# Performance work log

Measured on AMD Instinct MI355X. Metric: run time of the kernel, lower is better.

## Reference

```python
import jax, jax.numpy as jnp
import numpy as np

NUM_CODEBOOKS = 1
NUM_ENTRIES = 4096
ENTRY_DIM = 64


def setup_inputs() -> dict:
    key = jax.random.key(0)
    k1, k2 = jax.random.split(key)
    z = jax.random.normal(k1, (4, 1024, 8, 64), dtype=jnp.float32)
    weight = jax.random.normal(k2, (NUM_CODEBOOKS * NUM_ENTRIES, ENTRY_DIM), dtype=jnp.float32)
    return {"z": z, "weight": weight}


def _decode(z, weight):
    # Mirrors VQVAEQuantize.decode with cosine_distance=False.
    C, K, D = NUM_CODEBOOKS, NUM_ENTRIES, ENTRY_DIM
    input_shape = z.shape
    zf = z.reshape(-1, C, D).astype(jnp.float32)            # (N, C, D)
    cb = weight.reshape(C, K, D).astype(jnp.float32)        # (C, K, D)
    dots = jnp.einsum('ckd,ncd->cnk', cb, zf)               # (C, N, K)
    znorm = jnp.sum(zf * zf, axis=-1).T[:, :, None]         # (C, N, 1)
    cbnorm = jnp.sum(cb * cb, axis=-1)[:, None, :]          # (C, 1, K)
    sim = 2.0 * dots - znorm - cbnorm                        # negative squared dist
    idx = jnp.argmax(sim, axis=-1)                           # (C, N)
    idx = idx.T + jnp.arange(C, dtype=idx.dtype)[None, :] * K  # (N, C) global ids
    idx = idx.reshape(*input_shape[:-1], -1)
    z_q = weight[idx.reshape(-1)].reshape(input_shape)       # embedding gather
    return z_q, idx


def reference(z, weight):
    z_q, indices = _decode(z, weight)
    # commitment loss (training path): mse per (bsz, seq_len) position
    commitment_loss = ((z - jax.lax.stop_gradient(z_q)) ** 2)
    commitment_loss = commitment_loss.reshape(z.shape[0], z.shape[1], -1).mean(axis=-1)
    # codebook EMA statistics (update_codebook): one-hot scatter-add as segment_sum
    K_total = NUM_CODEBOOKS * NUM_ENTRIES
    flat_idx = indices.reshape(-1)
    encodings_sum = jax.ops.segment_sum(
        jnp.ones_like(flat_idx, dtype=jnp.float32), flat_idx, num_segments=K_total)
    embed_sum = jax.ops.segment_sum(
        z.reshape(-1, ENTRY_DIM), flat_idx, num_segments=K_total)
    # straight-through estimator (copy_grad=True)
    z_q = z + jax.lax.stop_gradient(z_q - z)
    return z_q, indices, commitment_loss, encodings_sum, embed_sum
```

## Files before the change

### kernel.cpp

```cpp
#include <hip/hip_runtime.h>
#include <math.h>

#define N_TOTAL   32768
#define K_ENT     4096
#define DIM       64
#define BM        64
#define BK        128
#define CAP       32
#define EPS       1.0f

typedef __attribute__((ext_vector_type(4))) float f32x4;
typedef __attribute__((ext_vector_type(8))) short bf16x8;
typedef __attribute__((ext_vector_type(4))) unsigned short u16x4;

#define WS_NCB    0
#define WS_WHI    4096
#define OUT_ZQ    0
#define OUT_IDX   2097152
#define OUT_LOSS  2129920
#define OUT_ENC   2134016
#define OUT_EMB   2138112

#define NEG_BIG   -3.0e38f

__device__ __forceinline__ float bf2f(unsigned short u) {
  return __uint_as_float(((unsigned int)u) << 16);
}
__device__ __forceinline__ unsigned short f2bf(float f) {
  unsigned int b = __float_as_uint(f);
  return (unsigned short)((b + 0x7fffu + ((b >> 16) & 1u)) >> 16);
}

__global__ __launch_bounds__(256) void negcbnorm_kernel(
    const float* __restrict__ w, float* __restrict__ ncb) {
  int k = blockIdx.x * 256 + threadIdx.x;
  const float4* p = (const float4*)(w + (size_t)k * DIM);
  float s = 0.f;
  #pragma unroll
  for (int i = 0; i < 16; ++i) {
    float4 v = p[i];
    s = fmaf(v.x, v.x, s); s = fmaf(v.y, v.y, s);
    s = fmaf(v.z, v.z, s); s = fmaf(v.w, v.w, s);
  }
  ncb[k] = -0.5f * s;
}

__global__ __launch_bounds__(256) void wsplit_kernel(
    const float* __restrict__ w, unsigned short* __restrict__ whi) {
  int i = blockIdx.x * 256 + threadIdx.x;
  float4 v = ((const float4*)w)[i];
  u16x4 h;
  h[0] = f2bf(v.x); h[1] = f2bf(v.y); h[2] = f2bf(v.z); h[3] = f2bf(v.w);
  ((u16x4*)whi)[i] = h;
}

__global__ __launch_bounds__(256, 2) void argmax_kernel(
    const float* __restrict__ z, const float* __restrict__ w,
    const unsigned short* __restrict__ whi,
    const float* __restrict__ ncb, float* __restrict__ out_idx) {
  __shared__ unsigned short wS[BK][DIM];
  __shared__ float pmax[BM][33];
  __shared__ float rowThr[BM];
  __shared__ int   cnt[BM];
  __shared__ int   cand[BM][CAP];

  const int tid = threadIdx.x;
  const int n0  = blockIdx.x * BM;
  const int wv  = tid >> 6;
  const int ln  = tid & 63;
  const int g   = ln >> 4;
  const int lm  = ln & 15;
  const int rb  = (wv & 1) * 32;
  const int eb  = (wv >> 1) * 64;

  bf16x8 ah[2][2];
  #pragma unroll
  for (int rt = 0; rt < 2; ++rt) {
    const float* zr = z + (size_t)(n0 + rb + rt * 16 + lm) * DIM;
    #pragma unroll
    for (int s = 0; s < 2; ++s) {
      float4 f0 = *(const float4*)(zr + s * 32 + g * 8);
      float4 f1 = *(const float4*)(zr + s * 32 + g * 8 + 4);
      float ff[8] = {f0.x, f0.y, f0.z, f0.w, f1.x, f1.y, f1.z, f1.w};
      bf16x8 h;
      #pragma unroll
      for (int i = 0; i < 8; ++i) h[i] = (short)f2bf(ff[i]);
      ah[rt][s] = h;
    }
  }

  float m[8];
  #pragma unroll
  for (int i = 0; i < 8; ++i) m[i] = NEG_BIG;

  for (int kc = 0; kc < K_ENT; kc += BK) {
    __syncthreads();
    #pragma unroll
    for (int it = 0; it < 4; ++it) {
      int u = it * 256 + tid;
      int e = u >> 3, gg = u & 7;
      bf16x8 hv = *(const bf16x8*)(whi + (size_t)(kc + e) * DIM + gg * 8);
      *(bf16x8*)&wS[e][(gg ^ (e & 7)) * 8] = hv;
    }
    __syncthreads();

    float nc[4];
    #pragma unroll
    for (int ct = 0; ct < 4; ++ct) nc[ct] = ncb[kc + eb + ct * 16 + lm];

    f32x4 acc[2][4];
    #pragma unroll
    for (int rt = 0; rt < 2; ++rt)
      #pragma unroll
      for (int ct = 0; ct < 4; ++ct)
        acc[rt][ct] = (f32x4){nc[ct], nc[ct], nc[ct], nc[ct]};

    #pragma unroll
    for (int ct = 0; ct < 4; ++ct) {
      const int e = eb + ct * 16 + lm;
      #pragma unroll
      for (int s = 0; s < 2; ++s) {
        const int sl = (s * 4 + g) ^ (e & 7);
        bf16x8 bh = *(const bf16x8*)&wS[e][sl * 8];
        #pragma unroll
        for (int rt = 0; rt < 2; ++rt)
          acc[rt][ct] = __builtin_amdgcn_mfma_f32_16x16x32_bf16(
              ah[rt][s], bh, acc[rt][ct], 0, 0, 0);
      }
    }

    #pragma unroll
    for (int rt = 0; rt < 2; ++rt)
      #pragma unroll
      for (int j = 0; j < 4; ++j) {
        const int so = rt * 4 + j;
        float t = fmaxf(fmaxf(acc[rt][0][j], acc[rt][1][j]), acc[rt][2][j]);
        m[so] = fmaxf(fmaxf(t, acc[rt][3][j]), m[so]);
      }
  }

  const int cw = (wv >> 1) * 16 + lm;
  #pragma unroll
  for (int rt = 0; rt < 2; ++rt)
    #pragma unroll
    for (int j = 0; j < 4; ++j)
      pmax[rb + rt * 16 + g * 4 + j][cw] = m[rt * 4 + j];
  __syncthreads();
  if (tid < BM) {
    float mm = NEG_BIG;
    for (int s = 0; s < 32; ++s) mm = fmaxf(mm, pmax[tid][s]);
    rowThr[tid] = mm - EPS;
    cnt[tid] = 0;
  }
  __syncthreads();

  float thr[8];
  #pragma unroll
  for (int rt = 0; rt < 2; ++rt)
    #pragma unroll
    for (int j = 0; j < 4; ++j)
      thr[rt * 4 + j] = rowThr[rb + rt * 16 + g * 4 + j];

  for (int kc = 0; kc < K_ENT; kc += BK) {
    __syncthreads();
    #pragma unroll
    for (int it = 0; it < 4; ++it) {
      int u = it * 256 + tid;
      int e = u >> 3, gg = u & 7;
      bf16x8 hv = *(const bf16x8*)(whi + (size_t)(kc + e) * DIM + gg * 8);
      *(bf16x8*)&wS[e][(gg ^ (e & 7)) * 8] = hv;
    }
    __syncthreads();

    float nc[4];
    #pragma unroll
    for (int ct = 0; ct < 4; ++ct) nc[ct] = ncb[kc + eb + ct * 16 + lm];

    f32x4 acc[2][4];
    #pragma unroll
    for (int rt = 0; rt < 2; ++rt)
      #pragma unroll
      for (int ct = 0; ct < 4; ++ct)
        acc[rt][ct] = (f32x4){nc[ct], nc[ct], nc[ct], nc[ct]};

    #pragma unroll
    for (int ct = 0; ct < 4; ++ct) {
      const int e = eb + ct * 16 + lm;
      #pragma unroll
      for (int s = 0; s < 2; ++s) {
        const int sl = (s * 4 + g) ^ (e & 7);
        bf16x8 bh = *(const bf16x8*)&wS[e][sl * 8];
        #pragma unroll
        for (int rt = 0; rt < 2; ++rt)
          acc[rt][ct] = __builtin_amdgcn_mfma_f32_16x16x32_bf16(
              ah[rt][s], bh, acc[rt][ct], 0, 0, 0);
      }
    }

    #pragma unroll
    for (int ct = 0; ct < 4; ++ct) {
      const int eg2 = kc + eb + ct * 16 + lm;
      #pragma unroll
      for (int rt = 0; rt < 2; ++rt)
        #pragma unroll
        for (int j = 0; j < 4; ++j) {
          float s = acc[rt][ct][j];
          if (__builtin_expect(s >= thr[rt * 4 + j], 0)) {
            int r = rb + rt * 16 + g * 4 + j;
            int p = atomicAdd(&cnt[r], 1);
            if (p < CAP) cand[r][p] = eg2;
          }
        }
    }
  }
  __syncthreads();

  if (tid < BM) {
    const int r = tid;
    int nn = cnt[r];
    nn = (nn > CAP) ? CAP : nn;
    const float* zr = z + (size_t)(n0 + r) * DIM;
    double best = -1.0e300;
    int win = 0;
    for (int p = 0; p < nn; ++p) {
      int c = cand[r][p];
      double td = 0.0, ud = 0.0;
      for (int d = 0; d < DIM; ++d) {
        double zv = (double)zr[d];
        double wv2 = (double)w[(size_t)c * DIM + d];
        td = fma(zv, wv2, td);
        ud = fma(wv2, wv2, ud);
      }
      double sd = 2.0 * td - ud;
      if (sd > best || (sd == best && c < win)) { best = sd; win = c; }
    }
    out_idx[n0 + r] = (float)win;
  }
}

__global__ __launch_bounds__(512) void gather_kernel(
    const float* __restrict__ z, const float* __restrict__ w,
    const float* __restrict__ idxf, float* __restrict__ out_zq,
    float* __restrict__ out_loss, float* __restrict__ enc,
    float* __restrict__ emb) {
  int bs = blockIdx.x;
  int tid = threadIdx.x;
  int h = tid >> 6, d = tid & 63;
  int n = bs * 8 + h;
  int k = (int)idxf[n];
  k = (k < 0) ? 0 : ((k > K_ENT - 1) ? (K_ENT - 1) : k);
  float zv = z[(size_t)n * DIM + d];
  float wv = w[(size_t)k * DIM + d];
  float st = zv + (wv - zv);
  out_zq[(size_t)n * DIM + d] = st;
  float diff = zv - wv;
  float s = diff * diff;
  #pragma unroll
  for (int mm = 32; mm >= 1; mm >>= 1) s += __shfl_down(s, mm, 64);
  __shared__ float red[8];
  if ((tid & 63) == 0) red[tid >> 6] = s;
  __syncthreads();
  if (tid == 0) {
    float t = 0.f;
    #pragma unroll
    for (int i = 0; i < 8; ++i) t += red[i];
    out_loss[bs] = t * (1.0f / 512.0f);
  }
  atomicAdd(&emb[(size_t)k * DIM + d], zv);
  if (d == 0) atomicAdd(&enc[k], 1.0f);
}

extern "C" void kernel_launch(void* const* d_in, const int* in_sizes, int n_in,
                              void* d_out, int out_size, void* d_ws, size_t ws_size,
                              hipStream_t stream) {
  const float* z = (const float*)d_in[0];
  const float* w = (const float*)d_in[1];
  float* ws  = (float*)d_ws;
  float* ncb = ws + WS_NCB;
  unsigned short* whi = (unsigned short*)(ws + WS_WHI);
  float* out = (float*)d_out;

  hipMemsetAsync(out + OUT_ENC, 0, (size_t)(4096 + 262144) * sizeof(float),
                 stream);

  negcbnorm_kernel<<<K_ENT / 256, 256, 0, stream>>>(w, ncb);
  wsplit_kernel<<<(K_ENT * DIM / 4) / 256, 256, 0, stream>>>(w, whi);
  argmax_kernel<<<N_TOTAL / BM, 256, 0, stream>>>(z, w, whi, ncb,
                                                  out + OUT_IDX);
  gather_kernel<<<N_TOTAL / 8, 512, 0, stream>>>(z, w, out + OUT_IDX,
                                                 out + OUT_ZQ, out + OUT_LOSS,
                                                 out + OUT_ENC, out + OUT_EMB);
}
```

Measured before the change: 127.6 us.

## Double-buffer codebook tiles in LDS with register prefetch in both passes

Both codebook scan passes now use two LDS buffers. Each iteration prefetches the next 128-entry bf16 tile and its norm values into registers before the MFMA work on the current tile, then stores them into the other buffer after the compute. This cuts the loop from two barriers to one and hides global-load latency behind the matrix math. In exchange it doubles the LDS used for the weight tile and adds registers for the prefetched data, which may reduce occupancy.

```diff
diff --git a/kernel.cpp b/kernel.cpp
--- a/kernel.cpp
+++ b/kernel.cpp
@@ -58,7 +58,7 @@
     const float* __restrict__ z, const float* __restrict__ w,
     const unsigned short* __restrict__ whi,
     const float* __restrict__ ncb, float* __restrict__ out_idx) {
-  __shared__ unsigned short wS[BK][DIM];
+  __shared__ unsigned short wS[2][BK][DIM];
   __shared__ float pmax[BM][33];
   __shared__ float rowThr[BM];
   __shared__ int   cnt[BM];
@@ -73,6 +73,9 @@
   const int rb  = (wv & 1) * 32;
   const int eb  = (wv >> 1) * 64;
 
+  const int se0 = tid >> 3;
+  const int sg  = tid & 7;
+
   bf16x8 ah[2][2];
   #pragma unroll
   for (int rt = 0; rt < 2; ++rt) {
@@ -93,27 +96,41 @@
   #pragma unroll
   for (int i = 0; i < 8; ++i) m[i] = NEG_BIG;
 
+  bf16x8 wpre[4];
+  float  ncc[4];
+  float  ncp[4];
+
+  #pragma unroll
+  for (int it = 0; it < 4; ++it)
+    wpre[it] = *(const bf16x8*)(whi + (size_t)(se0 + it * 32) * DIM + sg * 8);
+  #pragma unroll
+  for (int ct = 0; ct < 4; ++ct) ncc[ct] = ncb[eb + ct * 16 + lm];
+  #pragma unroll
+  for (int it = 0; it < 4; ++it) {
+    int e = se0 + it * 32;
+    *(bf16x8*)&wS[0][e][(sg ^ (e & 7)) * 8] = wpre[it];
+  }
+  __syncthreads();
+
   for (int kc = 0; kc < K_ENT; kc += BK) {
-    __syncthreads();
-    #pragma unroll
-    for (int it = 0; it < 4; ++it) {
-      int u = it * 256 + tid;
-      int e = u >> 3, gg = u & 7;
-      bf16x8 hv = *(const bf16x8*)(whi + (size_t)(kc + e) * DIM + gg * 8);
-      *(bf16x8*)&wS[e][(gg ^ (e & 7)) * 8] = hv;
-    }
-    __syncthreads();
-
-    float nc[4];
-    #pragma unroll
-    for (int ct = 0; ct < 4; ++ct) nc[ct] = ncb[kc + eb + ct * 16 + lm];
+    const int cur = (kc >> 7) & 1;
+    const bool more = (kc + BK) < K_ENT;
+    if (more) {
+      #pragma unroll
+      for (int it = 0; it < 4; ++it)
+        wpre[it] = *(const bf16x8*)(whi +
+                     (size_t)(kc + BK + se0 + it * 32) * DIM + sg * 8);
+      #pragma unroll
+      for (int ct = 0; ct < 4; ++ct)
+        ncp[ct] = ncb[kc + BK + eb + ct * 16 + lm];
+    }
 
     f32x4 acc[2][4];
     #pragma unroll
     for (int rt = 0; rt < 2; ++rt)
       #pragma unroll
       for (int ct = 0; ct < 4; ++ct)
-        acc[rt][ct] = (f32x4){nc[ct], nc[ct], nc[ct], nc[ct]};
+        acc[rt][ct] = (f32x4){ncc[ct], ncc[ct], ncc[ct], ncc[ct]};
 
     #pragma unroll
     for (int ct = 0; ct < 4; ++ct) {
@@ -121,7 +138,7 @@
       #pragma unroll
       for (int s = 0; s < 2; ++s) {
         const int sl = (s * 4 + g) ^ (e & 7);
-        bf16x8 bh = *(const bf16x8*)&wS[e][sl * 8];
+        bf16x8 bh = *(const bf16x8*)&wS[cur][e][sl * 8];
         #pragma unroll
         for (int rt = 0; rt < 2; ++rt)
           acc[rt][ct] = __builtin_amdgcn_mfma_f32_16x16x32_bf16(
@@ -137,6 +154,17 @@
         float t = fmaxf(fmaxf(acc[rt][0][j], acc[rt][1][j]), acc[rt][2][j]);
         m[so] = fmaxf(fmaxf(t, acc[rt][3][j]), m[so]);
       }
+
+    if (more) {
+      #pragma unroll
+      for (int it = 0; it < 4; ++it) {
+        int e = se0 + it * 32;
+        *(bf16x8*)&wS[cur ^ 1][e][(sg ^ (e & 7)) * 8] = wpre[it];
+      }
+      #pragma unroll
+      for (int ct = 0; ct < 4; ++ct) ncc[ct] = ncp[ct];
+    }
+    __syncthreads();
   }
 
   const int cw = (wv >> 1) * 16 + lm;
@@ -161,27 +189,37 @@
     for (int j = 0; j < 4; ++j)
       thr[rt * 4 + j] = rowThr[rb + rt * 16 + g * 4 + j];
 
+  #pragma unroll
+  for (int it = 0; it < 4; ++it)
+    wpre[it] = *(const bf16x8*)(whi + (size_t)(se0 + it * 32) * DIM + sg * 8);
+  #pragma unroll
+  for (int ct = 0; ct < 4; ++ct) ncc[ct] = ncb[eb + ct * 16 + lm];
+  #pragma unroll
+  for (int it = 0; it < 4; ++it) {
+    int e = se0 + it * 32;
+    *(bf16x8*)&wS[0][e][(sg ^ (e & 7)) * 8] = wpre[it];
+  }
+  __syncthreads();
+
   for (int kc = 0; kc < K_ENT; kc += BK) {
-    __syncthreads();
-    #pragma unroll
-    for (int it = 0; it < 4; ++it) {
-      int u = it * 256 + tid;
-      int e = u >> 3, gg = u & 7;
-      bf16x8 hv = *(const bf16x8*)(whi + (size_t)(kc + e) * DIM + gg * 8);
-      *(bf16x8*)&wS[e][(gg ^ (e & 7)) * 8] = hv;
-    }
-    __syncthreads();
-
-    float nc[4];
-    #pragma unroll
-    for (int ct = 0; ct < 4; ++ct) nc[ct] = ncb[kc + eb + ct * 16 + lm];
+    const int cur = (kc >> 7) & 1;
+    const bool more = (kc + BK) < K_ENT;
+    if (more) {
+      #pragma unroll
+      for (int it = 0; it < 4; ++it)
+        wpre[it] = *(const bf16x8*)(whi +
+                     (size_t)(kc + BK + se0 + it * 32) * DIM + sg * 8);
+      #pragma unroll
+      for (int ct = 0; ct < 4; ++ct)
+        ncp[ct] = ncb[kc + BK + eb + ct * 16 + lm];
+    }
 
     f32x4 acc[2][4];
     #pragma unroll
     for (int rt = 0; rt < 2; ++rt)
       #pragma unroll
       for (int ct = 0; ct < 4; ++ct)
-        acc[rt][ct] = (f32x4){nc[ct], nc[ct], nc[ct], nc[ct]};
+        acc[rt][ct] = (f32x4){ncc[ct], ncc[ct], ncc[ct], ncc[ct]};
 
     #pragma unroll
     for (int ct = 0; ct < 4; ++ct) {
@@ -189,7 +227,7 @@
       #pragma unroll
       for (int s = 0; s < 2; ++s) {
         const int sl = (s * 4 + g) ^ (e & 7);
-        bf16x8 bh = *(const bf16x8*)&wS[e][sl * 8];
+        bf16x8 bh = *(const bf16x8*)&wS[cur][e][sl * 8];
         #pragma unroll
         for (int rt = 0; rt < 2; ++rt)
           acc[rt][ct] = __builtin_amdgcn_mfma_f32_16x16x32_bf16(
@@ -212,8 +250,18 @@
           }
         }
     }
-  }
-  __syncthreads();
+
+    if (more) {
+      #pragma unroll
+      for (int it = 0; it < 4; ++it) {
+        int e = se0 + it * 32;
+        *(bf16x8*)&wS[cur ^ 1][e][(sg ^ (e & 7)) * 8] = wpre[it];
+      }
+      #pragma unroll
+      for (int ct = 0; ct < 4; ++ct) ncc[ct] = ncp[ct];
+    }
+    __syncthreads();
+  }
 
   if (tid < BM) {
     const int r = tid;
```

Measured after the change: 120.4 us. 1.06x faster.

## Stream codebook fragments directly from global into registers with double buffering

Applied to the files above, without the earlier changes.

The argmax kernel no longer stages codebook tiles through shared memory with block-wide barriers. Each wave now loads its own bf16 codebook fragments straight from global/L2 into registers, using two register buffers to overlap loads with MFMA work. Each wave also covers all 64 rows instead of 32, which doubles the A-fragment registers and the running-max state. Separately, the norm and bf16-conversion prep kernels are merged into one launch that uses a shuffle reduction. The trade-off is removed LDS traffic and syncs against more global/L2 loads per wave and higher register pressure.

```diff
diff --git a/kernel.cpp b/kernel.cpp
--- a/kernel.cpp
+++ b/kernel.cpp
@@ -31,35 +31,25 @@
   return (unsigned short)((b + 0x7fffu + ((b >> 16) & 1u)) >> 16);
 }
 
-__global__ __launch_bounds__(256) void negcbnorm_kernel(
-    const float* __restrict__ w, float* __restrict__ ncb) {
-  int k = blockIdx.x * 256 + threadIdx.x;
-  const float4* p = (const float4*)(w + (size_t)k * DIM);
-  float s = 0.f;
-  #pragma unroll
-  for (int i = 0; i < 16; ++i) {
-    float4 v = p[i];
-    s = fmaf(v.x, v.x, s); s = fmaf(v.y, v.y, s);
-    s = fmaf(v.z, v.z, s); s = fmaf(v.w, v.w, s);
-  }
-  ncb[k] = -0.5f * s;
-}
-
-__global__ __launch_bounds__(256) void wsplit_kernel(
-    const float* __restrict__ w, unsigned short* __restrict__ whi) {
+__global__ __launch_bounds__(256) void prep_kernel(
+    const float* __restrict__ w, unsigned short* __restrict__ whi,
+    float* __restrict__ ncb) {
   int i = blockIdx.x * 256 + threadIdx.x;
   float4 v = ((const float4*)w)[i];
   u16x4 h;
   h[0] = f2bf(v.x); h[1] = f2bf(v.y); h[2] = f2bf(v.z); h[3] = f2bf(v.w);
   ((u16x4*)whi)[i] = h;
+  float s = fmaf(v.x, v.x, fmaf(v.y, v.y, fmaf(v.z, v.z, v.w * v.w)));
+  s += __shfl_xor(s, 1); s += __shfl_xor(s, 2);
+  s += __shfl_xor(s, 4); s += __shfl_xor(s, 8);
+  if ((threadIdx.x & 15) == 0) ncb[i >> 4] = -0.5f * s;
 }
 
 __global__ __launch_bounds__(256, 2) void argmax_kernel(
     const float* __restrict__ z, const float* __restrict__ w,
     const unsigned short* __restrict__ whi,
     const float* __restrict__ ncb, float* __restrict__ out_idx) {
-  __shared__ unsigned short wS[BK][DIM];
-  __shared__ float pmax[BM][33];
+  __shared__ float pmax[BM][65];
   __shared__ float rowThr[BM];
   __shared__ int   cnt[BM];
   __shared__ int   cand[BM][CAP];
@@ -70,13 +60,12 @@
   const int ln  = tid & 63;
   const int g   = ln >> 4;
   const int lm  = ln & 15;
-  const int rb  = (wv & 1) * 32;
-  const int eb  = (wv >> 1) * 64;
-
-  bf16x8 ah[2][2];
-  #pragma unroll
-  for (int rt = 0; rt < 2; ++rt) {
-    const float* zr = z + (size_t)(n0 + rb + rt * 16 + lm) * DIM;
+  const int ecol = wv * 32 + lm;
+
+  bf16x8 ah[4][2];
+  #pragma unroll
+  for (int rt = 0; rt < 4; ++rt) {
+    const float* zr = z + (size_t)(n0 + rt * 16 + lm) * DIM;
     #pragma unroll
     for (int s = 0; s < 2; ++s) {
       float4 f0 = *(const float4*)(zr + s * 32 + g * 8);
@@ -89,129 +78,113 @@
     }
   }
 
-  float m[8];
-  #pragma unroll
-  for (int i = 0; i < 8; ++i) m[i] = NEG_BIG;
-
-  for (int kc = 0; kc < K_ENT; kc += BK) {
-    __syncthreads();
-    #pragma unroll
-    for (int it = 0; it < 4; ++it) {
-      int u = it * 256 + tid;
-      int e = u >> 3, gg = u & 7;
-      bf16x8 hv = *(const bf16x8*)(whi + (size_t)(kc + e) * DIM + gg * 8);
-      *(bf16x8*)&wS[e][(gg ^ (e & 7)) * 8] = hv;
-    }
-    __syncthreads();
-
-    float nc[4];
-    #pragma unroll
-    for (int ct = 0; ct < 4; ++ct) nc[ct] = ncb[kc + eb + ct * 16 + lm];
-
-    f32x4 acc[2][4];
-    #pragma unroll
-    for (int rt = 0; rt < 2; ++rt)
-      #pragma unroll
-      for (int ct = 0; ct < 4; ++ct)
+  bf16x8 bA[2][2], bB[2][2];
+  float  ncA[2], ncB[2];
+
+  auto loadB = [&](int kcb, bf16x8 (&bv)[2][2], float (&nc)[2]) {
+    #pragma unroll
+    for (int ct = 0; ct < 2; ++ct) {
+      const int ent = kcb + ecol + ct * 16;
+      nc[ct] = ncb[ent];
+      const unsigned short* wr = whi + (size_t)ent * DIM + g * 8;
+      bv[ct][0] = *(const bf16x8*)(wr);
+      bv[ct][1] = *(const bf16x8*)(wr + 32);
+    }
+  };
+
+  float m[16];
+  #pragma unroll
+  for (int i = 0; i < 16; ++i) m[i] = NEG_BIG;
+
+  auto comp1 = [&](const bf16x8 (&bv)[2][2], const float (&nc)[2]) {
+    f32x4 acc[4][2];
+    #pragma unroll
+    for (int rt = 0; rt < 4; ++rt)
+      #pragma unroll
+      for (int ct = 0; ct < 2; ++ct)
         acc[rt][ct] = (f32x4){nc[ct], nc[ct], nc[ct], nc[ct]};
-
-    #pragma unroll
-    for (int ct = 0; ct < 4; ++ct) {
-      const int e = eb + ct * 16 + lm;
-      #pragma unroll
-      for (int s = 0; s < 2; ++s) {
-        const int sl = (s * 4 + g) ^ (e & 7);
-        bf16x8 bh = *(const bf16x8*)&wS[e][sl * 8];
+    #pragma unroll
+    for (int ct = 0; ct < 2; ++ct)
+      #pragma unroll
+      for (int s = 0; s < 2; ++s)
         #pragma unroll
-        for (int rt = 0; rt < 2; ++rt)
+        for (int rt = 0; rt < 4; ++rt)
           acc[rt][ct] = __builtin_amdgcn_mfma_f32_16x16x32_bf16(
-              ah[rt][s], bh, acc[rt][ct], 0, 0, 0);
-      }
-    }
-
-    #pragma unroll
-    for (int rt = 0; rt < 2; ++rt)
-      #pragma unroll
-      for (int j = 0; j < 4; ++j) {
-        const int so = rt * 4 + j;
-        float t = fmaxf(fmaxf(acc[rt][0][j], acc[rt][1][j]), acc[rt][2][j]);
-        m[so] = fmaxf(fmaxf(t, acc[rt][3][j]), m[so]);
-      }
-  }
-
-  const int cw = (wv >> 1) * 16 + lm;
-  #pragma unroll
-  for (int rt = 0; rt < 2; ++rt)
+              ah[rt][s], bv[ct][s], acc[rt][ct], 0, 0, 0);
+    #pragma unroll
+    for (int rt = 0; rt < 4; ++rt)
+      #pragma unroll
+      for (int j = 0; j < 4; ++j)
+        m[rt * 4 + j] = fmaxf(fmaxf(acc[rt][0][j], acc[rt][1][j]),
+                              m[rt * 4 + j]);
+  };
+
+  loadB(0, bA, ncA);
+  for (int kc = 0; kc < K_ENT; kc += 2 * BK) {
+    loadB(kc + BK, bB, ncB);
+    comp1(bA, ncA);
+    if (kc + 2 * BK < K_ENT) loadB(kc + 2 * BK, bA, ncA);
+    comp1(bB, ncB);
+  }
+
+  #pragma unroll
+  for (int rt = 0; rt < 4; ++rt)
     #pragma unroll
     for (int j = 0; j < 4; ++j)
-      pmax[rb + rt * 16 + g * 4 + j][cw] = m[rt * 4 + j];
+      pmax[rt * 16 + g * 4 + j][wv * 16 + lm] = m[rt * 4 + j];
   __syncthreads();
   if (tid < BM) {
     float mm = NEG_BIG;
-    for (int s = 0; s < 32; ++s) mm = fmaxf(mm, pmax[tid][s]);
+    for (int s = 0; s < 64; ++s) mm = fmaxf(mm, pmax[tid][s]);
     rowThr[tid] = mm - EPS;
     cnt[tid] = 0;
   }
   __syncthreads();
 
-  float thr[8];
-  #pragma unroll
-  for (int rt = 0; rt < 2; ++rt)
+  float thr[16];
+  #pragma unroll
+  for (int rt = 0; rt < 4; ++rt)
     #pragma unroll
     for (int j = 0; j < 4; ++j)
-      thr[rt * 4 + j] = rowThr[rb + rt * 16 + g * 4 + j];
-
-  for (int kc = 0; kc < K_ENT; kc += BK) {
-    __syncthreads();
-    #pragma unroll
-    for (int it = 0; it < 4; ++it) {
-      int u = it * 256 + tid;
-      int e = u >> 3, gg = u & 7;
-      bf16x8 hv = *(const bf16x8*)(whi + (size_t)(kc + e) * DIM + gg * 8);
-      *(bf16x8*)&wS[e][(gg ^ (e & 7)) * 8] = hv;
-    }
-    __syncthreads();
-
-    float nc[4];
-    #pragma unroll
-    for (int ct = 0; ct < 4; ++ct) nc[ct] = ncb[kc + eb + ct * 16 + lm];
-
-    f32x4 acc[2][4];
-    #pragma unroll
-    for (int rt = 0; rt < 2; ++rt)
-      #pragma unroll
-      for (int ct = 0; ct < 4; ++ct)
+      thr[rt * 4 + j] = rowThr[rt * 16 + g * 4 + j];
+
+  auto comp2 = [&](int kcb, const bf16x8 (&bv)[2][2], const float (&nc)[2]) {
+    f32x4 acc[4][2];
+    #pragma unroll
+    for (int rt = 0; rt < 4; ++rt)
+      #pragma unroll
+      for (int ct = 0; ct < 2; ++ct)
         acc[rt][ct] = (f32x4){nc[ct], nc[ct], nc[ct], nc[ct]};
-
-    #pragma unroll
-    for (int ct = 0; ct < 4; ++ct) {
-      const int e = eb + ct * 16 + lm;
-      #pragma unroll
-      for (int s = 0; s < 2; ++s) {
-        const int sl = (s * 4 + g) ^ (e & 7);
-        bf16x8 bh = *(const bf16x8*)&wS[e][sl * 8];
+    #pragma unroll
+    for (int ct = 0; ct < 2; ++ct)
+      #pragma unroll
+      for (int s = 0; s < 2; ++s)
         #pragma unroll
-        for (int rt = 0; rt < 2; ++rt)
+        for (int rt = 0; rt < 4; ++rt)
           acc[rt][ct] = __builtin_amdgcn_mfma_f32_16x16x32_bf16(
-              ah[rt][s], bh, acc[rt][ct], 0, 0, 0);
-      }
-    }
-
-    #pragma unroll
-    for (int ct = 0; ct < 4; ++ct) {
-      const int eg2 = kc + eb + ct * 16 + lm;
-      #pragma unroll
-      for (int rt = 0; rt < 2; ++rt)
+              ah[rt][s], bv[ct][s], acc[rt][ct], 0, 0, 0);
+    #pragma unroll
+    for (int ct = 0; ct < 2; ++ct) {
+      const int eg2 = kcb + ecol + ct * 16;
+      #pragma unroll
+      for (int rt = 0; rt < 4; ++rt)
         #pragma unroll
         for (int j = 0; j < 4; ++j) {
-          float s = acc[rt][ct][j];
-          if (__builtin_expect(s >= thr[rt * 4 + j], 0)) {
-            int r = rb + rt * 16 + g * 4 + j;
+          if (__builtin_expect(acc[rt][ct][j] >= thr[rt * 4 + j], 0)) {
+            int r = rt * 16 + g * 4 + j;
             int p = atomicAdd(&cnt[r], 1);
             if (p < CAP) cand[r][p] = eg2;
           }
         }
     }
+  };
+
+  loadB(0, bA, ncA);
+  for (int kc = 0; kc < K_ENT; kc += 2 * BK) {
+    loadB(kc + BK, bB, ncB);
+    comp2(kc, bA, ncA);
+    if (kc + 2 * BK < K_ENT) loadB(kc + 2 * BK, bA, ncA);
+    comp2(kc + BK, bB, ncB);
   }
   __syncthreads();
 
@@ -283,8 +256,7 @@
   hipMemsetAsync(out + OUT_ENC, 0, (size_t)(4096 + 262144) * sizeof(float),
                  stream);
 
-  negcbnorm_kernel<<<K_ENT / 256, 256, 0, stream>>>(w, ncb);
-  wsplit_kernel<<<(K_ENT * DIM / 4) / 256, 256, 0, stream>>>(w, whi);
+  prep_kernel<<<(K_ENT * DIM / 4) / 256, 256, 0, stream>>>(w, whi, ncb);
   argmax_kernel<<<N_TOTAL / BM, 256, 0, stream>>>(z, w, whi, ncb,
                                                   out + OUT_IDX);
   gather_kernel<<<N_TOTAL / 8, 512, 0, stream>>>(z, w, out + OUT_IDX,
```

New measurement: 113.5 us. 11.1% less time.
